# Kernel optimization log

Hardware: AMD Instinct MI355X
Metric: run time of the kernel (lower is better)

## Reference

```python
import jax, jax.numpy as jnp
import numpy as np

T, B, H, D = 128, 8, 8, 64


def setup_inputs() -> dict:
    key = jax.random.key(0)
    kA, kB, kS = jax.random.split(key, 3)
    # Gated-delta transition matrices: near-identity contractions so the
    # length-T matrix-product recurrence is numerically stable, mimicking
    # A_t = gamma_t * (I - beta_t k_t k_t^T) of the gated delta rule.
    eye = jnp.eye(D, dtype=jnp.float32)
    A = 0.9 * eye + 0.06 * jax.random.normal(kA, (T, B, H, D, D), dtype=jnp.float32)
    Bm = jax.random.normal(kB, (T, B, H, D, D), dtype=jnp.float32)
    init_state = jax.random.normal(kS, (B, H, D, D), dtype=jnp.float32)
    return {"A": A, "Bm": Bm, "init_state": init_state}


def reference(A, Bm, init_state):
    """Gated delta rule recurrence S_t = S_{t-1} @ A_t + B_t for all t,
    computed with a parallel associative scan (Blelloch-equivalent).

    A:  [T,B,H,D,D] transition matrices
    Bm: [T,B,H,D,D] additive updates
    init_state: [B,H,D,D]
    returns states: [T,B,H,D,D]
    """
    def combine(e1, e2):
        # apply e1 first, then e2:
        # (S A1 + B1) A2 + B2 = S (A1 A2) + (B1 A2 + B2)
        A1, B1 = e1
        A2, B2 = e2
        A12 = jnp.einsum('tbhij,tbhjk->tbhik', A1, A2)
        B12 = jnp.einsum('tbhij,tbhjk->tbhik', B1, A2) + B2
        return (A12, B12)

    cumA, cumB = jax.lax.associative_scan(combine, (A, Bm), axis=0)
    # S_t = init_state @ cumA_t + cumB_t
    states = jnp.einsum('bhij,tbhjk->tbhik', init_state, cumA) + cumB
    return states
```

## Files before the change

kernel.cpp:

```cpp
#include <hip/hip_runtime.h>


constexpr int kT = 128;
constexpr int kBH = 64;
constexpr int kD = 64;
constexpr int kTile = kD * kD;
constexpr int kNC = 16;
constexpr int kCH = 8;

typedef __attribute__((ext_vector_type(8))) short short8;
typedef __attribute__((ext_vector_type(4))) float f32x4;
using u32 = unsigned int;

union U8 { u32 u[4]; short8 s; };

__device__ __forceinline__ void softBarrier() {
  asm volatile("s_waitcnt lgkmcnt(0)" ::: "memory");
  __builtin_amdgcn_s_barrier();
}

__device__ __forceinline__ int swzi(int r, int c) { return (r * 64 + c) ^ ((r & 7) << 3); }

__device__ __forceinline__ f32x4 mfma16(short8 a, short8 b, f32x4 c) {
  return __builtin_amdgcn_mfma_f32_16x16x32_bf16(a, b, c, 0, 0, 0);
}

__device__ __forceinline__ void pk_split(float a, float b, u32& h, u32& l) {
  u32 hu;
  asm("v_cvt_pk_bf16_f32 %0, %1, %2" : "=v"(hu) : "v"(a), "v"(b));
  const float ra = a - __uint_as_float(hu << 16);
  const float rb = b - __uint_as_float(hu & 0xffff0000u);
  u32 lu;
  asm("v_cvt_pk_bf16_f32 %0, %1, %2" : "=v"(lu) : "v"(ra), "v"(rb));
  h = hu;
  l = lu;
}

__device__ __forceinline__ short8 gather_frag(u32 p01, u32 p23, u32 q01, u32 q23,
                                              int ad0, int ad1, bool lowh) {
  U8 r;
  int x, y;
  x = __builtin_amdgcn_ds_bpermute(ad0, (int)p01);
  y = __builtin_amdgcn_ds_bpermute(ad0, (int)q01);
  r.u[0] = (u32)(lowh ? x : y);
  x = __builtin_amdgcn_ds_bpermute(ad0, (int)p23);
  y = __builtin_amdgcn_ds_bpermute(ad0, (int)q23);
  r.u[1] = (u32)(lowh ? x : y);
  x = __builtin_amdgcn_ds_bpermute(ad1, (int)p01);
  y = __builtin_amdgcn_ds_bpermute(ad1, (int)q01);
  r.u[2] = (u32)(lowh ? x : y);
  x = __builtin_amdgcn_ds_bpermute(ad1, (int)p23);
  y = __builtin_amdgcn_ds_bpermute(ad1, (int)q23);
  r.u[3] = (u32)(lowh ? x : y);
  return r.s;
}

#define STAGE_A(AH, AL, BUFA)                                            \
  do {                                                                   \
    _Pragma("unroll") for (int s_ = 0; s_ < 2; ++s_) {                   \
      U8 h_, l_;                                                         \
      _Pragma("unroll") for (int p_ = 0; p_ < 4; ++p_) {                 \
        u32 hu_, lu_;                                                    \
        pk_split(BUFA[s_ * 8 + 2 * p_], BUFA[s_ * 8 + 2 * p_ + 1], hu_, lu_); \
        h_.u[p_] = hu_;                                                  \
        l_.u[p_] = lu_;                                                  \
      }                                                                  \
      const int idx_ = swzi(lane, w * 16 + s_ * 8);                      \
      *reinterpret_cast<short8*>(&(AH)[idx_]) = h_.s;                    \
      *reinterpret_cast<short8*>(&(AL)[idx_]) = l_.s;                    \
    }                                                                    \
  } while (0)

#define LOAD_A(BUFA, ptr)                                                \
  do {                                                                   \
    const float* At_ = (ptr);                                            \
    _Pragma("unroll") for (int kk_ = 0; kk_ < 16; ++kk_)                 \
        BUFA[kk_] = At_[(w * 16 + kk_) * 64 + lane];                     \
  } while (0)

#define LOAD_B(BUFB, ptr)                                                \
  do {                                                                   \
    const float* Bt_ = (ptr);                                            \
    _Pragma("unroll") for (int cm_ = 0; cm_ < 4; ++cm_)                  \
        BUFB[cm_] = *reinterpret_cast<const f32x4*>(Bt_ + rowbase + cm_ * 16 + q * 4); \
  } while (0)

#define FOLD_STEP(J, CUR, BUFA)                                               \
  do {                                                                        \
    const int j_ = (J);                                                       \
    const bool more_ = (j_ + 1 < nS);                                         \
    f32x4 npa[4], npb[4];                                                     \
    _Pragma("unroll") for (int cm = 0; cm < 4; ++cm) {                        \
      npa[cm] = (f32x4){0.f, 0.f, 0.f, 0.f};                                  \
      npb[cm] = bufB[cm];                                                     \
    }                                                                         \
    if (j_ + 2 <= eMax)                                                       \
      LOAD_B(bufB, srcB + (size_t)(e0 + (long)(j_ + 2) * elemStride) * kTile);\
    if (more_) {                                                              \
      STAGE_A(sAh[(CUR) ^ 1], sAl[(CUR) ^ 1], BUFA);                          \
      if (j_ + 4 <= eMax)                                                     \
        LOAD_A(BUFA, srcA + (size_t)(e0 + (long)(j_ + 4) * elemStride) * kTile);\
    }                                                                         \
    _Pragma("unroll") for (int ks = 0; ks < 2; ++ks) {                        \
      u32 pa01h, pa01l, pa23h, pa23l, qa01h, qa01l, qa23h, qa23l;             \
      u32 pb01h, pb01l, pb23h, pb23l, qb01h, qb01l, qb23h, qb23l;             \
      pk_split(apa[2 * ks][0], apa[2 * ks][1], pa01h, pa01l);                 \
      pk_split(apa[2 * ks][2], apa[2 * ks][3], pa23h, pa23l);                 \
      pk_split(apa[2 * ks + 1][0], apa[2 * ks + 1][1], qa01h, qa01l);         \
      pk_split(apa[2 * ks + 1][2], apa[2 * ks + 1][3], qa23h, qa23l);         \
      pk_split(apb[2 * ks][0], apb[2 * ks][1], pb01h, pb01l);                 \
      pk_split(apb[2 * ks][2], apb[2 * ks][3], pb23h, pb23l);                 \
      pk_split(apb[2 * ks + 1][0], apb[2 * ks + 1][1], qb01h, qb01l);         \
      pk_split(apb[2 * ks + 1][2], apb[2 * ks + 1][3], qb23h, qb23l);         \
      const short8 bah = gather_frag(pa01h, pa23h, qa01h, qa23h, ad0, ad1, lowh); \
      const short8 bal = gather_frag(pa01l, pa23l, qa01l, qa23l, ad0, ad1, lowh); \
      const short8 bbh = gather_frag(pb01h, pb23h, qb01h, qb23h, ad0, ad1, lowh); \
      const short8 bbl = gather_frag(pb01l, pb23l, qb01l, qb23l, ad0, ad1, lowh); \
      _Pragma("unroll") for (int cm = 0; cm < 4; ++cm) {                      \
        const int ai = swzi(cm * 16 + l15, ks * 32 + q * 8);                  \
        const short8 ah = *reinterpret_cast<const short8*>(&sAh[(CUR)][ai]);  \
        const short8 al = *reinterpret_cast<const short8*>(&sAl[(CUR)][ai]);  \
        npa[cm] = mfma16(ah, bah, npa[cm]);                                   \
        npa[cm] = mfma16(ah, bal, npa[cm]);                                   \
        npa[cm] = mfma16(al, bah, npa[cm]);                                   \
        npb[cm] = mfma16(ah, bbh, npb[cm]);                                   \
        npb[cm] = mfma16(ah, bbl, npb[cm]);                                   \
        npb[cm] = mfma16(al, bbh, npb[cm]);                                   \
      }                                                                       \
    }                                                                         \
    _Pragma("unroll") for (int cm = 0; cm < 4; ++cm) {                        \
      apa[cm] = npa[cm];                                                      \
      apb[cm] = npb[cm];                                                      \
    }                                                                         \
    if (more_) softBarrier();                                                 \
  } while (0)

__global__ __launch_bounds__(256, 4) void gdr_fold(
    const float* __restrict__ srcA, const float* __restrict__ srcB,
    float* __restrict__ dstA, float* __restrict__ dstB,
    int perChain, long chainBase, long idxBase, long elemStride, int nElem) {
  __shared__ unsigned short sAh[2][4096], sAl[2][4096];

  const int tid = threadIdx.x;
  const int lane = tid & 63, w = tid >> 6;
  const int q = lane >> 4, l15 = lane & 15;
  const int bh = blockIdx.x / perChain, id = blockIdx.x % perChain;
  const long e0 = (long)bh * chainBase + (long)id * idxBase;
  const int rowbase = (w * 16 + l15) * 64;
  const int ad0 = (l15 + ((lane >> 4) & 1) * 32) * 4;
  const int ad1 = ad0 + 64;
  const bool lowh = lane < 32;
  const int nS = nElem - 1;
  const int eMax = nElem - 1;

  auto clampE = [&](int e) { return e < eMax ? e : eMax; };

  f32x4 apa[4], apb[4];
  {
    const float* At = srcA + (size_t)e0 * kTile;
    const float* Bt = srcB + (size_t)e0 * kTile;
#pragma unroll
    for (int cm = 0; cm < 4; ++cm) {
      apa[cm] = *reinterpret_cast<const f32x4*>(At + rowbase + cm * 16 + q * 4);
      apb[cm] = *reinterpret_cast<const f32x4*>(Bt + rowbase + cm * 16 + q * 4);
    }
  }

  float bufA0[16], bufA1[16];
  f32x4 bufB[4];
  LOAD_A(bufA0, srcA + (size_t)(e0 + (long)clampE(1) * elemStride) * kTile);
  LOAD_B(bufB, srcB + (size_t)(e0 + (long)clampE(1) * elemStride) * kTile);
  LOAD_A(bufA1, srcA + (size_t)(e0 + (long)clampE(3) * elemStride) * kTile);
  STAGE_A(sAh[0], sAl[0], bufA0);
  LOAD_A(bufA0, srcA + (size_t)(e0 + (long)clampE(2) * elemStride) * kTile);
  softBarrier();

  int j = 0;
  while (true) {
    FOLD_STEP(j, 0, bufA0);
    if (++j >= nS) break;
    FOLD_STEP(j, 1, bufA1);
    if (++j >= nS) break;
  }

  float* pao = dstA + (size_t)blockIdx.x * kTile;
  float* pbo = dstB + (size_t)blockIdx.x * kTile;
#pragma unroll
  for (int cm = 0; cm < 4; ++cm) {
    *reinterpret_cast<f32x4*>(pao + rowbase + cm * 16 + q * 4) = apa[cm];
    *reinterpret_cast<f32x4*>(pbo + rowbase + cm * 16 + q * 4) = apb[cm];
  }
}

#define SCAN_STEP(I, CUR, BUFA)                                               \
  do {                                                                        \
    const int i_ = (I);                                                       \
    const bool more_ = (i_ + 1 < nSteps);                                     \
    f32x4 nacc[4];                                                            \
    _Pragma("unroll") for (int cm = 0; cm < 4; ++cm) nacc[cm] = bufB[cm];     \
    if (i_ + 1 <= eMax)                                                       \
      LOAD_B(bufB, srcB + (size_t)(e0 + (long)(i_ + 1) * elemStride) * kTile);\
    if (more_) {                                                              \
      STAGE_A(sAh[(CUR) ^ 1], sAl[(CUR) ^ 1], BUFA);                          \
      if (i_ + 3 <= eMax)                                                     \
        LOAD_A(BUFA, srcA + (size_t)(e0 + (long)(i_ + 3) * elemStride) * kTile);\
    }                                                                         \
    _Pragma("unroll") for (int ks = 0; ks < 2; ++ks) {                        \
      u32 p01h, p01l, p23h, p23l, q01h, q01l, q23h, q23l;                     \
      pk_split(acc[2 * ks][0], acc[2 * ks][1], p01h, p01l);                   \
      pk_split(acc[2 * ks][2], acc[2 * ks][3], p23h, p23l);                   \
      pk_split(acc[2 * ks + 1][0], acc[2 * ks + 1][1], q01h, q01l);           \
      pk_split(acc[2 * ks + 1][2], acc[2 * ks + 1][3], q23h, q23l);           \
      const short8 bfh = gather_frag(p01h, p23h, q01h, q23h, ad0, ad1, lowh); \
      const short8 bfl = gather_frag(p01l, p23l, q01l, q23l, ad0, ad1, lowh); \
      _Pragma("unroll") for (int cm = 0; cm < 4; ++cm) {                      \
        const int ai = swzi(cm * 16 + l15, ks * 32 + q * 8);                  \
        const short8 ah = *reinterpret_cast<const short8*>(&sAh[(CUR)][ai]);  \
        const short8 al = *reinterpret_cast<const short8*>(&sAl[(CUR)][ai]);  \
        nacc[cm] = mfma16(ah, bfh, nacc[cm]);                                 \
        nacc[cm] = mfma16(ah, bfl, nacc[cm]);                                 \
        nacc[cm] = mfma16(al, bfh, nacc[cm]);                                 \
      }                                                                       \
    }                                                                         \
    const int t_ = tBase + (i_ + 1) * tStep - 1;                              \
    float* o_ = out + ((size_t)t_ * kBH + bh) * kTile;                        \
    _Pragma("unroll") for (int cm = 0; cm < 4; ++cm) {                        \
      *reinterpret_cast<f32x4*>(o_ + rowbase + cm * 16 + q * 4) = nacc[cm];   \
      acc[cm] = nacc[cm];                                                     \
    }                                                                         \
    if (more_) softBarrier();                                                 \
  } while (0)

__global__ __launch_bounds__(256, 4) void gdr_scan(
    const float* __restrict__ srcA, const float* __restrict__ srcB,
    const float* __restrict__ S0, float* __restrict__ out,
    int perChain, long chainBase, long idxBase, long elemStride,
    int nSteps, int tbMul, int tStep) {
  __shared__ unsigned short sAh[2][4096], sAl[2][4096];

  const int tid = threadIdx.x;
  const int lane = tid & 63, w = tid >> 6;
  const int q = lane >> 4, l15 = lane & 15;
  const int bh = blockIdx.x / perChain, id = blockIdx.x % perChain;
  const long e0 = (long)bh * chainBase + (long)id * idxBase;
  const int tBase = id * tbMul;
  const int rowbase = (w * 16 + l15) * 64;
  const int ad0 = (l15 + ((lane >> 4) & 1) * 32) * 4;
  const int ad1 = ad0 + 64;
  const bool lowh = lane < 32;
  const int eMax = nSteps - 1;

  auto clampE = [&](int e) { return e < eMax ? e : eMax; };

  f32x4 acc[4];
  {
    const float* Sb = (tBase == 0) ? (S0 + (size_t)bh * kTile)
                                   : (out + ((size_t)(tBase - 1) * kBH + bh) * kTile);
#pragma unroll
    for (int cm = 0; cm < 4; ++cm)
      acc[cm] = *reinterpret_cast<const f32x4*>(Sb + rowbase + cm * 16 + q * 4);
  }

  float bufA0[16], bufA1[16];
  f32x4 bufB[4];
  LOAD_A(bufA0, srcA + (size_t)e0 * kTile);
  LOAD_B(bufB, srcB + (size_t)e0 * kTile);
  LOAD_A(bufA1, srcA + (size_t)(e0 + (long)clampE(2) * elemStride) * kTile);
  STAGE_A(sAh[0], sAl[0], bufA0);
  LOAD_A(bufA0, srcA + (size_t)(e0 + (long)clampE(1) * elemStride) * kTile);
  softBarrier();

  int i = 0;
  while (true) {
    SCAN_STEP(i, 0, bufA0);
    if (++i >= nSteps) break;
    SCAN_STEP(i, 1, bufA1);
    if (++i >= nSteps) break;
  }
}

extern "C" void kernel_launch(void* const* d_in, const int* in_sizes, int n_in,
                              void* d_out, int out_size, void* d_ws, size_t ws_size,
                              hipStream_t stream) {
  const float* A  = (const float*)d_in[0];
  const float* Bm = (const float*)d_in[1];
  const float* S0 = (const float*)d_in[2];
  float* out = (float*)d_out;

  float* PA = (float*)d_ws;
  float* PB = PA + (size_t)kBH * kNC * kTile;

  gdr_fold<<<dim3(kBH * kNC), dim3(256), 0, stream>>>(
      A, Bm, PA, PB, kNC, 1L, (long)kCH * kBH, (long)kBH, kCH);
  gdr_scan<<<dim3(kBH), dim3(256), 0, stream>>>(
      PA, PB, S0, out, 1, (long)kNC, 0L, 1L, kNC, 0, kCH);
  gdr_scan<<<dim3(kBH * kNC), dim3(256), 0, stream>>>(
      A, Bm, S0, out, kNC, 1L, (long)kCH * kBH, (long)kBH, kCH - 1, kCH, 1);
}
```

Baseline: 185.8 us.

## Stream A tiles directly into LDS via global_load_lds and split on read

Replaces the register-staged A pipeline (load to registers, split to bf16 hi/lo, write to swizzled LDS) with direct global-to-LDS async loads of fp32 A tiles into a double buffer. The bf16 hi/lo split now happens on each read from LDS. The aim is to cut register pressure and VGPR staging work and to overlap the loads with MFMA. In exchange it doubles LDS footprint per element, repeats the split work on every fragment read, and shortens the prefetch distance from several steps ahead to one.

Measured after the change: 317.1 us. 70.7% more time.

```diff
diff --git a/kernel.cpp b/kernel.cpp
--- a/kernel.cpp
+++ b/kernel.cpp
@@ -13,13 +13,6 @@
 using u32 = unsigned int;
 
 union U8 { u32 u[4]; short8 s; };
-
-__device__ __forceinline__ void softBarrier() {
-  asm volatile("s_waitcnt lgkmcnt(0)" ::: "memory");
-  __builtin_amdgcn_s_barrier();
-}
-
-__device__ __forceinline__ int swzi(int r, int c) { return (r * 64 + c) ^ ((r & 7) << 3); }
 
 __device__ __forceinline__ f32x4 mfma16(short8 a, short8 b, f32x4 c) {
   return __builtin_amdgcn_mfma_f32_16x16x32_bf16(a, b, c, 0, 0, 0);
@@ -55,52 +48,53 @@
   return r.s;
 }
 
-#define STAGE_A(AH, AL, BUFA)                                            \
-  do {                                                                   \
-    _Pragma("unroll") for (int s_ = 0; s_ < 2; ++s_) {                   \
-      U8 h_, l_;                                                         \
-      _Pragma("unroll") for (int p_ = 0; p_ < 4; ++p_) {                 \
-        u32 hu_, lu_;                                                    \
-        pk_split(BUFA[s_ * 8 + 2 * p_], BUFA[s_ * 8 + 2 * p_ + 1], hu_, lu_); \
-        h_.u[p_] = hu_;                                                  \
-        l_.u[p_] = lu_;                                                  \
-      }                                                                  \
-      const int idx_ = swzi(lane, w * 16 + s_ * 8);                      \
-      *reinterpret_cast<short8*>(&(AH)[idx_]) = h_.s;                    \
-      *reinterpret_cast<short8*>(&(AL)[idx_]) = l_.s;                    \
-    }                                                                    \
-  } while (0)
-
-#define LOAD_A(BUFA, ptr)                                                \
-  do {                                                                   \
-    const float* At_ = (ptr);                                            \
-    _Pragma("unroll") for (int kk_ = 0; kk_ < 16; ++kk_)                 \
-        BUFA[kk_] = At_[(w * 16 + kk_) * 64 + lane];                     \
-  } while (0)
-
-#define LOAD_B(BUFB, ptr)                                                \
-  do {                                                                   \
-    const float* Bt_ = (ptr);                                            \
-    _Pragma("unroll") for (int cm_ = 0; cm_ < 4; ++cm_)                  \
-        BUFB[cm_] = *reinterpret_cast<const f32x4*>(Bt_ + rowbase + cm_ * 16 + q * 4); \
-  } while (0)
-
-#define FOLD_STEP(J, CUR, BUFA)                                               \
+__device__ __forceinline__ void read_afrag(const float* sAbuf, int row, int k0,
+                                           short8& ah, short8& al) {
+  const int m = (row & 7) << 2;
+  const f32x4 x = *reinterpret_cast<const f32x4*>(&sAbuf[row * 64 + (k0 ^ m)]);
+  const f32x4 y = *reinterpret_cast<const f32x4*>(&sAbuf[row * 64 + ((k0 + 4) ^ m)]);
+  U8 h, l;
+  u32 hu, lu;
+  pk_split(x[0], x[1], hu, lu); h.u[0] = hu; l.u[0] = lu;
+  pk_split(x[2], x[3], hu, lu); h.u[1] = hu; l.u[1] = lu;
+  pk_split(y[0], y[1], hu, lu); h.u[2] = hu; l.u[2] = lu;
+  pk_split(y[2], y[3], hu, lu); h.u[3] = hu; l.u[3] = lu;
+  ah = h.s; al = l.s;
+}
+
+#define ISSUE_A(PTRA, SBUF)                                                   \
+  do {                                                                        \
+    const char* gb_ = (const char*)(PTRA);                                    \
+    _Pragma("unroll") for (int it_ = 0; it_ < 16; ++it_) {                    \
+      __builtin_amdgcn_global_load_lds(                                       \
+          (const __attribute__((address_space(1))) u32*)(gb_ + aoff[it_]),    \
+          (__attribute__((address_space(3))) u32*)&(SBUF)[(w * 16 + it_) * 64], \
+          4, 0, 0);                                                           \
+    }                                                                         \
+    __builtin_amdgcn_sched_barrier(0);                                        \
+  } while (0)
+
+#define LOAD_B4(PTRB)                                                          \
+  do {                                                                         \
+    const float* Bt_ = (PTRB);                                                 \
+    b0 = *reinterpret_cast<const f32x4*>(Bt_ + rowbase + 0 * 16 + q * 4);      \
+    b1 = *reinterpret_cast<const f32x4*>(Bt_ + rowbase + 1 * 16 + q * 4);      \
+    b2 = *reinterpret_cast<const f32x4*>(Bt_ + rowbase + 2 * 16 + q * 4);      \
+    b3 = *reinterpret_cast<const f32x4*>(Bt_ + rowbase + 3 * 16 + q * 4);      \
+  } while (0)
+
+#define FOLD_STEP(J, SCUR, SNXT)                                              \
   do {                                                                        \
     const int j_ = (J);                                                       \
     const bool more_ = (j_ + 1 < nS);                                         \
+    if (more_)                                                                \
+      ISSUE_A(srcA + (size_t)(e0 + (long)(j_ + 2) * elemStride) * kTile, SNXT); \
     f32x4 npa[4], npb[4];                                                     \
-    _Pragma("unroll") for (int cm = 0; cm < 4; ++cm) {                        \
-      npa[cm] = (f32x4){0.f, 0.f, 0.f, 0.f};                                  \
-      npb[cm] = bufB[cm];                                                     \
-    }                                                                         \
-    if (j_ + 2 <= eMax)                                                       \
-      LOAD_B(bufB, srcB + (size_t)(e0 + (long)(j_ + 2) * elemStride) * kTile);\
-    if (more_) {                                                              \
-      STAGE_A(sAh[(CUR) ^ 1], sAl[(CUR) ^ 1], BUFA);                          \
-      if (j_ + 4 <= eMax)                                                     \
-        LOAD_A(BUFA, srcA + (size_t)(e0 + (long)(j_ + 4) * elemStride) * kTile);\
-    }                                                                         \
+    npb[0] = b0; npb[1] = b1; npb[2] = b2; npb[3] = b3;                       \
+    _Pragma("unroll") for (int cm = 0; cm < 4; ++cm)                          \
+        npa[cm] = (f32x4){0.f, 0.f, 0.f, 0.f};                                \
+    if (more_)                                                                \
+      LOAD_B4(srcB + (size_t)(e0 + (long)(j_ + 2) * elemStride) * kTile);     \
     _Pragma("unroll") for (int ks = 0; ks < 2; ++ks) {                        \
       u32 pa01h, pa01l, pa23h, pa23l, qa01h, qa01l, qa23h, qa23l;             \
       u32 pb01h, pb01l, pb23h, pb23l, qb01h, qb01l, qb23h, qb23l;             \
@@ -117,9 +111,8 @@
       const short8 bbh = gather_frag(pb01h, pb23h, qb01h, qb23h, ad0, ad1, lowh); \
       const short8 bbl = gather_frag(pb01l, pb23l, qb01l, qb23l, ad0, ad1, lowh); \
       _Pragma("unroll") for (int cm = 0; cm < 4; ++cm) {                      \
-        const int ai = swzi(cm * 16 + l15, ks * 32 + q * 8);                  \
-        const short8 ah = *reinterpret_cast<const short8*>(&sAh[(CUR)][ai]);  \
-        const short8 al = *reinterpret_cast<const short8*>(&sAl[(CUR)][ai]);  \
+        short8 ah, al;                                                        \
+        read_afrag(&(SCUR)[0], cm * 16 + l15, ks * 32 + q * 8, ah, al);       \
         npa[cm] = mfma16(ah, bah, npa[cm]);                                   \
         npa[cm] = mfma16(ah, bal, npa[cm]);                                   \
         npa[cm] = mfma16(al, bah, npa[cm]);                                   \
@@ -132,14 +125,14 @@
       apa[cm] = npa[cm];                                                      \
       apb[cm] = npb[cm];                                                      \
     }                                                                         \
-    if (more_) softBarrier();                                                 \
+    if (more_) __syncthreads();                                               \
   } while (0)
 
 __global__ __launch_bounds__(256, 4) void gdr_fold(
     const float* __restrict__ srcA, const float* __restrict__ srcB,
     float* __restrict__ dstA, float* __restrict__ dstB,
     int perChain, long chainBase, long idxBase, long elemStride, int nElem) {
-  __shared__ unsigned short sAh[2][4096], sAl[2][4096];
+  __shared__ float sA0[4096], sA1[4096];
 
   const int tid = threadIdx.x;
   const int lane = tid & 63, w = tid >> 6;
@@ -151,9 +144,13 @@
   const int ad1 = ad0 + 64;
   const bool lowh = lane < 32;
   const int nS = nElem - 1;
-  const int eMax = nElem - 1;
-
-  auto clampE = [&](int e) { return e < eMax ? e : eMax; };
+
+  int aoff[16];
+#pragma unroll
+  for (int it = 0; it < 16; ++it) {
+    const int n = w * 16 + it;
+    aoff[it] = (((lane ^ ((n & 7) << 2)) << 6) + n) * 4;
+  }
 
   f32x4 apa[4], apb[4];
   {
@@ -166,20 +163,16 @@
     }
   }
 
-  float bufA0[16], bufA1[16];
-  f32x4 bufB[4];
-  LOAD_A(bufA0, srcA + (size_t)(e0 + (long)clampE(1) * elemStride) * kTile);
-  LOAD_B(bufB, srcB + (size_t)(e0 + (long)clampE(1) * elemStride) * kTile);
-  LOAD_A(bufA1, srcA + (size_t)(e0 + (long)clampE(3) * elemStride) * kTile);
-  STAGE_A(sAh[0], sAl[0], bufA0);
-  LOAD_A(bufA0, srcA + (size_t)(e0 + (long)clampE(2) * elemStride) * kTile);
-  softBarrier();
+  f32x4 b0, b1, b2, b3;
+  ISSUE_A(srcA + (size_t)(e0 + elemStride) * kTile, sA0);
+  LOAD_B4(srcB + (size_t)(e0 + elemStride) * kTile);
+  __syncthreads();
 
   int j = 0;
   while (true) {
-    FOLD_STEP(j, 0, bufA0);
+    FOLD_STEP(j, sA0, sA1);
     if (++j >= nS) break;
-    FOLD_STEP(j, 1, bufA1);
+    FOLD_STEP(j, sA1, sA0);
     if (++j >= nS) break;
   }
 
@@ -192,19 +185,16 @@
   }
 }
 
-#define SCAN_STEP(I, CUR, BUFA)                                               \
+#define SCAN_STEP(I, SCUR, SNXT)                                              \
   do {                                                                        \
     const int i_ = (I);                                                       \
     const bool more_ = (i_ + 1 < nSteps);                                     \
+    if (more_)                                                                \
+      ISSUE_A(srcA + (size_t)(e0 + (long)(i_ + 1) * elemStride) * kTile, SNXT); \
     f32x4 nacc[4];                                                            \
-    _Pragma("unroll") for (int cm = 0; cm < 4; ++cm) nacc[cm] = bufB[cm];     \
-    if (i_ + 1 <= eMax)                                                       \
-      LOAD_B(bufB, srcB + (size_t)(e0 + (long)(i_ + 1) * elemStride) * kTile);\
-    if (more_) {                                                              \
-      STAGE_A(sAh[(CUR) ^ 1], sAl[(CUR) ^ 1], BUFA);                          \
-      if (i_ + 3 <= eMax)                                                     \
-        LOAD_A(BUFA, srcA + (size_t)(e0 + (long)(i_ + 3) * elemStride) * kTile);\
-    }                                                                         \
+    nacc[0] = b0; nacc[1] = b1; nacc[2] = b2; nacc[3] = b3;                   \
+    if (more_)                                                                \
+      LOAD_B4(srcB + (size_t)(e0 + (long)(i_ + 1) * elemStride) * kTile);     \
     _Pragma("unroll") for (int ks = 0; ks < 2; ++ks) {                        \
       u32 p01h, p01l, p23h, p23l, q01h, q01l, q23h, q23l;                     \
       pk_split(acc[2 * ks][0], acc[2 * ks][1], p01h, p01l);                   \
@@ -214,9 +204,8 @@
       const short8 bfh = gather_frag(p01h, p23h, q01h, q23h, ad0, ad1, lowh); \
       const short8 bfl = gather_frag(p01l, p23l, q01l, q23l, ad0, ad1, lowh); \
       _Pragma("unroll") for (int cm = 0; cm < 4; ++cm) {                      \
-        const int ai = swzi(cm * 16 + l15, ks * 32 + q * 8);                  \
-        const short8 ah = *reinterpret_cast<const short8*>(&sAh[(CUR)][ai]);  \
-        const short8 al = *reinterpret_cast<const short8*>(&sAl[(CUR)][ai]);  \
+        short8 ah, al;                                                        \
+        read_afrag(&(SCUR)[0], cm * 16 + l15, ks * 32 + q * 8, ah, al);       \
         nacc[cm] = mfma16(ah, bfh, nacc[cm]);                                 \
         nacc[cm] = mfma16(ah, bfl, nacc[cm]);                                 \
         nacc[cm] = mfma16(al, bfh, nacc[cm]);                                 \
@@ -228,7 +217,7 @@
       *reinterpret_cast<f32x4*>(o_ + rowbase + cm * 16 + q * 4) = nacc[cm];   \
       acc[cm] = nacc[cm];                                                     \
     }                                                                         \
-    if (more_) softBarrier();                                                 \
+    if (more_) __syncthreads();                                               \
   } while (0)
 
 __global__ __launch_bounds__(256, 4) void gdr_scan(
@@ -236,7 +225,7 @@
     const float* __restrict__ S0, float* __restrict__ out,
     int perChain, long chainBase, long idxBase, long elemStride,
     int nSteps, int tbMul, int tStep) {
-  __shared__ unsigned short sAh[2][4096], sAl[2][4096];
+  __shared__ float sA0[4096], sA1[4096];
 
   const int tid = threadIdx.x;
   const int lane = tid & 63, w = tid >> 6;
@@ -248,9 +237,13 @@
   const int ad0 = (l15 + ((lane >> 4) & 1) * 32) * 4;
   const int ad1 = ad0 + 64;
   const bool lowh = lane < 32;
-  const int eMax = nSteps - 1;
-
-  auto clampE = [&](int e) { return e < eMax ? e : eMax; };
+
+  int aoff[16];
+#pragma unroll
+  for (int it = 0; it < 16; ++it) {
+    const int n = w * 16 + it;
+    aoff[it] = (((lane ^ ((n & 7) << 2)) << 6) + n) * 4;
+  }
 
   f32x4 acc[4];
   {
@@ -261,20 +254,16 @@
       acc[cm] = *reinterpret_cast<const f32x4*>(Sb + rowbase + cm * 16 + q * 4);
   }
 
-  float bufA0[16], bufA1[16];
-  f32x4 bufB[4];
-  LOAD_A(bufA0, srcA + (size_t)e0 * kTile);
-  LOAD_B(bufB, srcB + (size_t)e0 * kTile);
-  LOAD_A(bufA1, srcA + (size_t)(e0 + (long)clampE(2) * elemStride) * kTile);
-  STAGE_A(sAh[0], sAl[0], bufA0);
-  LOAD_A(bufA0, srcA + (size_t)(e0 + (long)clampE(1) * elemStride) * kTile);
-  softBarrier();
+  f32x4 b0, b1, b2, b3;
+  ISSUE_A(srcA + (size_t)e0 * kTile, sA0);
+  LOAD_B4(srcB + (size_t)e0 * kTile);
+  __syncthreads();
 
   int i = 0;
   while (true) {
-    SCAN_STEP(i, 0, bufA0);
+    SCAN_STEP(i, sA0, sA1);
     if (++i >= nSteps) break;
-    SCAN_STEP(i, 1, bufA1);
+    SCAN_STEP(i, sA1, sA0);
     if (++i >= nSteps) break;
   }
 }
```
